# Kernel optimization log

Hardware: AMD Instinct MI355X
Metric: run time of the kernel (lower is better)

The kernel has to match this reference:

```python
import jax, jax.numpy as jnp
import numpy as np

B, S, H = 4, 2048, 2048
I = 1408          # expert intermediate size
E = 8             # num_experts
K = 2             # num_experts_per_tok


def setup_inputs() -> dict:
    key = jax.random.key(0)
    ks = jax.random.split(key, 5)
    sc_h = 1.0 / np.sqrt(H)
    sc_i = 1.0 / np.sqrt(I)
    return {
        "hidden_states": jax.random.normal(ks[0], (B, S, H), dtype=jnp.float32),
        "gate_w": jax.random.normal(ks[1], (E, H), dtype=jnp.float32) * sc_h,      # router: Linear(H, E)
        "w_gate": jax.random.normal(ks[2], (E, H, I), dtype=jnp.float32) * sc_h,   # experts_gate_proj
        "w_up": jax.random.normal(ks[3], (E, H, I), dtype=jnp.float32) * sc_h,     # experts_up_proj
        "w_down": jax.random.normal(ks[4], (E, I, H), dtype=jnp.float32) * sc_i,   # experts_down_proj
    }


def reference(hidden_states, gate_w, w_gate, w_up, w_down):
    b, s, h = hidden_states.shape
    x = hidden_states.reshape(-1, h)                       # [T, H], T = b*s
    # Router: softmax over experts, then top-k and renormalize (matches torch code).
    router_logits = x @ gate_w.T                           # [T, E]
    routing_weights = jax.nn.softmax(router_logits, axis=-1)
    topk_w, topk_i = jax.lax.top_k(routing_weights, K)     # [T, K]
    topk_w = topk_w / jnp.sum(topk_w, axis=-1, keepdims=True)
    out = jnp.zeros_like(x)
    # Loop over the small fixed expert set; tokens not routed to expert e get
    # combine weight 0, so their contribution vanishes (same math as masked gather).
    for e in range(w_gate.shape[0]):
        w_e = jnp.sum(jnp.where(topk_i == e, topk_w, 0.0), axis=-1)  # [T]
        gated = jax.nn.silu(x @ w_gate[e]) * (x @ w_up[e])           # [T, I]
        out = out + w_e[:, None] * (gated @ w_down[e])               # [T, H]
    return out.reshape(b, s, h)
```

## Files before the change

### kernel.cpp

```cpp
#include <hip/hip_runtime.h>

#define T_TOK 8192
#define H_DIM 2048
#define I_DIM 1408
#define N_EXP 8
#define MAX_TILES 144
#define R_BLOCKS 512

typedef __attribute__((ext_vector_type(8))) short short8;
typedef __attribute__((ext_vector_type(8))) unsigned short ushort8;
typedef __attribute__((ext_vector_type(4))) float f32x4;


__device__ __forceinline__ unsigned short f2bf(float f) {
  unsigned u = __float_as_uint(f);
  u += 0x7fffu + ((u >> 16) & 1u);
  return (unsigned short)(u >> 16);
}
__device__ __forceinline__ float bf2f(unsigned short u) {
  return __uint_as_float(((unsigned)u) << 16);
}

__device__ __forceinline__ void g2lds16(const unsigned short* g, unsigned short* l) {
  __builtin_amdgcn_global_load_lds(
      (const __attribute__((address_space(1))) void*)g,
      (__attribute__((address_space(3))) void*)l, 16, 0, 0);
}

__global__ __launch_bounds__(256) void router_kernel(
    const float* __restrict__ X, const float* __restrict__ GW,
    int* __restrict__ topk_e, float* __restrict__ topk_p,
    int* __restrict__ counts_blk, unsigned short* __restrict__ Xb) {
  int wave = threadIdx.x >> 6, lane = threadIdx.x & 63;
  __shared__ int hist[8];
  if (threadIdx.x < 8) hist[threadIdx.x] = 0;
  __syncthreads();

  int tok0 = blockIdx.x * 16 + wave * 4;
  const float4* g4 = (const float4*)GW;
  const float4* x4 = (const float4*)X;

  float acc[4][8];
#pragma unroll
  for (int t = 0; t < 4; t++)
#pragma unroll
    for (int e = 0; e < 8; e++) acc[t][e] = 0.f;

#pragma unroll
  for (int i = 0; i < 8; i++) {
    float4 gv[8];
#pragma unroll
    for (int e = 0; e < 8; e++) gv[e] = g4[e * 512 + lane + i * 64];
#pragma unroll
    for (int t = 0; t < 4; t++) {
      float4 xv = x4[(size_t)(tok0 + t) * 512 + lane + i * 64];
      ushort4 o;
      o.x = f2bf(xv.x); o.y = f2bf(xv.y); o.z = f2bf(xv.z); o.w = f2bf(xv.w);
      *(ushort4*)(Xb + (size_t)(tok0 + t) * H_DIM + (size_t)(lane + i * 64) * 4) = o;
#pragma unroll
      for (int e = 0; e < 8; e++)
        acc[t][e] += xv.x * gv[e].x + xv.y * gv[e].y + xv.z * gv[e].z + xv.w * gv[e].w;
    }
  }

#pragma unroll
  for (int t = 0; t < 4; t++) {
#pragma unroll
    for (int e = 0; e < 8; e++) {
      float v = acc[t][e];
      for (int off = 32; off; off >>= 1) v += __shfl_down(v, off);
      acc[t][e] = v;
    }
    if (lane == 0) {
      int token = tok0 + t;
      int e1 = 0; float l1 = acc[t][0];
#pragma unroll
      for (int e = 1; e < 8; e++) if (acc[t][e] > l1) { l1 = acc[t][e]; e1 = e; }
      int e2 = -1; float l2 = -1e30f;
#pragma unroll
      for (int e = 0; e < 8; e++) if (e != e1 && acc[t][e] > l2) { l2 = acc[t][e]; e2 = e; }
      float tt = __expf(l2 - l1);
      float p1 = 1.f / (1.f + tt);
      float p2 = tt / (1.f + tt);
      topk_e[token * 2] = e1; topk_e[token * 2 + 1] = e2;
      topk_p[token * 2] = p1; topk_p[token * 2 + 1] = p2;
      atomicAdd(&hist[e1], 1);
      atomicAdd(&hist[e2], 1);
    }
  }
  __syncthreads();
  if (threadIdx.x < 8) counts_blk[blockIdx.x * 8 + threadIdx.x] = hist[threadIdx.x];
}

__global__ __launch_bounds__(256) void setup_kernel(
    const int* __restrict__ counts_blk, int* __restrict__ cursor,
    int* __restrict__ ntiles, int* __restrict__ tile_e,
    int* __restrict__ tile_b, int* __restrict__ tile_r) {
  __shared__ int scnt[8];
  __shared__ int off[9], tb[9], cnt[8];
  int t = threadIdx.x, lane = t & 63;
  if (t < 8) scnt[t] = 0;
  __syncthreads();

  int priv[8];
#pragma unroll
  for (int e = 0; e < 8; e++) priv[e] = 0;
  for (int b = t; b < R_BLOCKS; b += 256) {
#pragma unroll
    for (int e = 0; e < 8; e++) priv[e] += counts_blk[b * 8 + e];
  }
#pragma unroll
  for (int e = 0; e < 8; e++)
    for (int o = 32; o; o >>= 1) priv[e] += __shfl_down(priv[e], o);
  if (lane == 0) {
#pragma unroll
    for (int e = 0; e < 8; e++) atomicAdd(&scnt[e], priv[e]);
  }
  __syncthreads();

  if (t == 0) {
    int o = 0, nt = 0;
    for (int e = 0; e < N_EXP; e++) {
      int n = scnt[e];
      cnt[e] = n; off[e] = o; tb[e] = nt;
      cursor[e] = o;
      nt += (n + 127) >> 7;
      o += n;
    }
    off[8] = o; tb[8] = nt;
    *ntiles = nt;
  }
  __syncthreads();
  int total = tb[8];
  for (int i = t; i < total; i += 256) {
    int e = 0;
    while (i >= tb[e + 1]) e++;
    int k = i - tb[e];
    tile_e[i] = e;
    tile_b[i] = off[e] + k * 128;
    int rem = cnt[e] - k * 128;
    tile_r[i] = rem < 128 ? rem : 128;
  }
}

__global__ __launch_bounds__(256) void scatter_kernel(
    const int* __restrict__ topk_e, int* __restrict__ cursor,
    int* __restrict__ pair_tok, int* __restrict__ slot) {
  __shared__ int lcnt[8], lbase[8];
  int tid = threadIdx.x;
  if (tid < 8) lcnt[tid] = 0;
  __syncthreads();
  int tok = blockIdx.x * 256 + tid;
  int e0 = topk_e[tok * 2], e1 = topk_e[tok * 2 + 1];
  int p0 = atomicAdd(&lcnt[e0], 1);
  int p1 = atomicAdd(&lcnt[e1], 1);
  __syncthreads();
  if (tid < 8) lbase[tid] = atomicAdd(&cursor[tid], lcnt[tid]);
  __syncthreads();
  int s0 = lbase[e0] + p0, s1 = lbase[e1] + p1;
  pair_tok[s0] = tok;
  pair_tok[s1] = tok;
  slot[tok * 2] = s0;
  slot[tok * 2 + 1] = s1;
}

__global__ __launch_bounds__(256) void transpose_cvt_kernel(
    const float* __restrict__ in, unsigned short* __restrict__ out, int R, int C) {
  __shared__ float S[64][65];
  int e = blockIdx.z;
  int c0 = blockIdx.x * 64, r0 = blockIdx.y * 64;
  const float* ine = in + (size_t)e * R * C;
  unsigned short* oute = out + (size_t)e * R * C;
  int t = threadIdx.x;
  int li = (t & 15) * 4, lr = t >> 4;
#pragma unroll
  for (int p = 0; p < 4; p++) {
    int r = lr + p * 16;
    float4 v = *(const float4*)(ine + (size_t)(r0 + r) * C + c0 + li);
    S[r][li] = v.x; S[r][li + 1] = v.y; S[r][li + 2] = v.z; S[r][li + 3] = v.w;
  }
  __syncthreads();
  int c = t >> 2, q = t & 3;
#pragma unroll
  for (int i = 0; i < 2; i++) {
    int rb = i * 32 + q * 8;
    ushort8 o;
#pragma unroll
    for (int j = 0; j < 8; j++) o[j] = f2bf(S[rb + j][c]);
    *(ushort8*)(oute + (size_t)(c0 + c) * R + r0 + rb) = o;
  }
}

__global__ __launch_bounds__(256, 2) void gemm1_kernel(
    const unsigned short* __restrict__ Xb, const unsigned short* __restrict__ Wgt,
    const unsigned short* __restrict__ Wut, const int* __restrict__ ntiles,
    const int* __restrict__ tile_e, const int* __restrict__ tile_b,
    const int* __restrict__ tile_r, const int* __restrict__ pair_tok,
    unsigned short* __restrict__ G, int tile_base) {
  int bx = blockIdx.y + tile_base;
  if (bx >= *ntiles) return;
  int e = tile_e[bx], mbase = tile_b[bx], rows = tile_r[bx];
  int n0 = blockIdx.x * 128;
  int tid = threadIdx.x, wave = tid >> 6, lane = tid & 63;
  int quad = lane >> 4, c = lane & 15;
  int wm = (wave & 1) * 64, wn = (wave >> 1) * 64;

  __shared__ __align__(16) unsigned short As[2][128][32];
  __shared__ __align__(16) unsigned short Bgs[2][128][32];
  __shared__ __align__(16) unsigned short Bus[2][128][32];

  int srow = wave * 32 + (lane >> 2);
  int selem = (lane & 3) * 8;
  int mr0 = srow < rows ? srow : 0;
  int mr1 = (srow + 16) < rows ? (srow + 16) : 0;
  const unsigned short* gA0 = Xb + (size_t)pair_tok[mbase + mr0] * H_DIM + selem;
  const unsigned short* gA1 = Xb + (size_t)pair_tok[mbase + mr1] * H_DIM + selem;
  const unsigned short* bg = Wgt + (size_t)e * H_DIM * I_DIM;
  const unsigned short* bu = Wut + (size_t)e * H_DIM * I_DIM;
  const unsigned short* gG0 = bg + (size_t)(n0 + srow) * H_DIM + selem;
  const unsigned short* gG1 = bg + (size_t)(n0 + srow + 16) * H_DIM + selem;
  const unsigned short* gU0 = bu + (size_t)(n0 + srow) * H_DIM + selem;
  const unsigned short* gU1 = bu + (size_t)(n0 + srow + 16) * H_DIM + selem;

  f32x4 accg[4][4], accu[4][4];
#pragma unroll
  for (int i = 0; i < 4; i++)
#pragma unroll
    for (int j = 0; j < 4; j++) { accg[i][j] = (f32x4)0.f; accu[i][j] = (f32x4)0.f; }

  for (int k0 = 0; k0 < H_DIM; k0 += 64) {
    __syncthreads();
#pragma unroll
    for (int s = 0; s < 2; s++) {
      int kk = k0 + s * 32;
      g2lds16(gA0 + kk, &As[s][wave * 32][0]);
      g2lds16(gA1 + kk, &As[s][wave * 32 + 16][0]);
      g2lds16(gG0 + kk, &Bgs[s][wave * 32][0]);
      g2lds16(gG1 + kk, &Bgs[s][wave * 32 + 16][0]);
      g2lds16(gU0 + kk, &Bus[s][wave * 32][0]);
      g2lds16(gU1 + kk, &Bus[s][wave * 32 + 16][0]);
    }
    __syncthreads();

#pragma unroll
    for (int h = 0; h < 2; h++) {
      short8 af[4], bgf[4], buf[4];
#pragma unroll
      for (int mt = 0; mt < 4; mt++)
        af[mt] = *(const short8*)&As[h][wm + mt * 16 + c][quad * 8];
#pragma unroll
      for (int nt = 0; nt < 4; nt++) {
        bgf[nt] = *(const short8*)&Bgs[h][wn + nt * 16 + c][quad * 8];
        buf[nt] = *(const short8*)&Bus[h][wn + nt * 16 + c][quad * 8];
      }
#pragma unroll
      for (int mt = 0; mt < 4; mt++)
#pragma unroll
        for (int nt = 0; nt < 4; nt++) {
          accg[mt][nt] = __builtin_amdgcn_mfma_f32_16x16x32_bf16(af[mt], bgf[nt], accg[mt][nt], 0, 0, 0);
          accu[mt][nt] = __builtin_amdgcn_mfma_f32_16x16x32_bf16(af[mt], buf[nt], accu[mt][nt], 0, 0, 0);
        }
    }
  }

#pragma unroll
  for (int mt = 0; mt < 4; mt++)
#pragma unroll
    for (int r = 0; r < 4; r++) {
      int m = wm + mt * 16 + quad * 4 + r;
      if (m < rows) {
        unsigned short* grow = G + (size_t)(mbase + m) * I_DIM + n0 + wn;
#pragma unroll
        for (int nt = 0; nt < 4; nt++) {
          float g = accg[mt][nt][r], u = accu[mt][nt][r];
          float val = (g / (1.f + __expf(-g))) * u;
          grow[nt * 16 + c] = f2bf(val);
        }
      }
    }
}

__global__ __launch_bounds__(256, 3) void gemm2_kernel(
    const unsigned short* __restrict__ G, const unsigned short* __restrict__ Wdt,
    const int* __restrict__ ntiles, const int* __restrict__ tile_e,
    const int* __restrict__ tile_b, const int* __restrict__ tile_r,
    unsigned short* __restrict__ Y) {
  int bx = blockIdx.y;
  if (bx >= *ntiles) return;
  int e = tile_e[bx], mbase = tile_b[bx], rows = tile_r[bx];
  int n0 = blockIdx.x * 128;
  int tid = threadIdx.x, wave = tid >> 6, lane = tid & 63;
  int quad = lane >> 4, c = lane & 15;
  int wm = (wave & 1) * 64, wn = (wave >> 1) * 64;

  __shared__ __align__(16) unsigned short As[2][128][32];
  __shared__ __align__(16) unsigned short Bs[2][128][32];

  int srow = wave * 32 + (lane >> 2);
  int selem = (lane & 3) * 8;
  int mr0 = srow < rows ? srow : 0;
  int mr1 = (srow + 16) < rows ? (srow + 16) : 0;
  const unsigned short* gA0 = G + (size_t)(mbase + mr0) * I_DIM + selem;
  const unsigned short* gA1 = G + (size_t)(mbase + mr1) * I_DIM + selem;
  const unsigned short* bd = Wdt + (size_t)e * H_DIM * I_DIM;
  const unsigned short* gB0 = bd + (size_t)(n0 + srow) * I_DIM + selem;
  const unsigned short* gB1 = bd + (size_t)(n0 + srow + 16) * I_DIM + selem;

  f32x4 acc[4][4];
#pragma unroll
  for (int i = 0; i < 4; i++)
#pragma unroll
    for (int j = 0; j < 4; j++) acc[i][j] = (f32x4)0.f;

  for (int k0 = 0; k0 < I_DIM; k0 += 64) {
    __syncthreads();
#pragma unroll
    for (int s = 0; s < 2; s++) {
      int kk = k0 + s * 32;
      g2lds16(gA0 + kk, &As[s][wave * 32][0]);
      g2lds16(gA1 + kk, &As[s][wave * 32 + 16][0]);
      g2lds16(gB0 + kk, &Bs[s][wave * 32][0]);
      g2lds16(gB1 + kk, &Bs[s][wave * 32 + 16][0]);
    }
    __syncthreads();

#pragma unroll
    for (int h = 0; h < 2; h++) {
      short8 af[4], bf[4];
#pragma unroll
      for (int mt = 0; mt < 4; mt++)
        af[mt] = *(const short8*)&As[h][wm + mt * 16 + c][quad * 8];
#pragma unroll
      for (int nt = 0; nt < 4; nt++)
        bf[nt] = *(const short8*)&Bs[h][wn + nt * 16 + c][quad * 8];
#pragma unroll
      for (int mt = 0; mt < 4; mt++)
#pragma unroll
        for (int nt = 0; nt < 4; nt++)
          acc[mt][nt] = __builtin_amdgcn_mfma_f32_16x16x32_bf16(af[mt], bf[nt], acc[mt][nt], 0, 0, 0);
    }
  }

#pragma unroll
  for (int mt = 0; mt < 4; mt++)
#pragma unroll
    for (int r = 0; r < 4; r++) {
      int m = wm + mt * 16 + quad * 4 + r;
      if (m < rows) {
        unsigned short* yrow = Y + (size_t)(mbase + m) * H_DIM + n0 + wn;
#pragma unroll
        for (int nt = 0; nt < 4; nt++) yrow[nt * 16 + c] = f2bf(acc[mt][nt][r]);
      }
    }
}

__global__ __launch_bounds__(256) void combine_kernel(
    const unsigned short* __restrict__ Y, const int* __restrict__ slot,
    const float* __restrict__ topk_p, float* __restrict__ out) {
  int t = blockIdx.x;
  int h = threadIdx.x * 8;
  int s1 = slot[t * 2], s2 = slot[t * 2 + 1];
  float p1 = topk_p[t * 2], p2 = topk_p[t * 2 + 1];
  ushort8 a = *(const ushort8*)(Y + (size_t)s1 * H_DIM + h);
  ushort8 b = *(const ushort8*)(Y + (size_t)s2 * H_DIM + h);
  float* o = out + (size_t)t * H_DIM + h;
  float4 o0, o1;
  o0.x = p1 * bf2f(a[0]) + p2 * bf2f(b[0]);
  o0.y = p1 * bf2f(a[1]) + p2 * bf2f(b[1]);
  o0.z = p1 * bf2f(a[2]) + p2 * bf2f(b[2]);
  o0.w = p1 * bf2f(a[3]) + p2 * bf2f(b[3]);
  o1.x = p1 * bf2f(a[4]) + p2 * bf2f(b[4]);
  o1.y = p1 * bf2f(a[5]) + p2 * bf2f(b[5]);
  o1.z = p1 * bf2f(a[6]) + p2 * bf2f(b[6]);
  o1.w = p1 * bf2f(a[7]) + p2 * bf2f(b[7]);
  *(float4*)o = o0;
  *(float4*)(o + 4) = o1;
}

extern "C" void kernel_launch(void* const* d_in, const int* in_sizes, int n_in,
                              void* d_out, int out_size, void* d_ws, size_t ws_size,
                              hipStream_t stream) {
  const float* X  = (const float*)d_in[0];
  const float* GW = (const float*)d_in[1];
  const float* Wg = (const float*)d_in[2];
  const float* Wu = (const float*)d_in[3];
  const float* Wd = (const float*)d_in[4];
  float* out = (float*)d_out;

  char* ws = (char*)d_ws;
  int*   cursor   = (int*)(ws + 32);
  int*   ntiles   = (int*)(ws + 64);
  int*   tile_e   = (int*)(ws + 128);
  int*   tile_b   = (int*)(ws + 1280);
  int*   tile_r   = (int*)(ws + 2432);
  int*   topk_e   = (int*)(ws + 4096);
  float* topk_p   = (float*)(ws + 69632);
  int*   pair_tok = (int*)(ws + 135168);
  int*   slot     = (int*)(ws + 200704);
  int*   counts_blk = (int*)(ws + 200704);
  unsigned short* Xb  = (unsigned short*)(ws + 266240);
  unsigned short* G   = (unsigned short*)(ws + 33820672);
  unsigned short* Wgt = (unsigned short*)(ws + 79958016);
  unsigned short* Wut = (unsigned short*)(ws + 126095360);
  unsigned short* Wdt = (unsigned short*)(ws + 172232704);
  unsigned short* Y   = (unsigned short*)(ws + 79958016);


  router_kernel<<<R_BLOCKS, 256, 0, stream>>>(X, GW, topk_e, topk_p, counts_blk, Xb);
  setup_kernel<<<1, 256, 0, stream>>>(counts_blk, cursor, ntiles, tile_e, tile_b, tile_r);
  scatter_kernel<<<T_TOK / 256, 256, 0, stream>>>(topk_e, cursor, pair_tok, slot);
  transpose_cvt_kernel<<<dim3(I_DIM / 64, H_DIM / 64, N_EXP), 256, 0, stream>>>(Wg, Wgt, H_DIM, I_DIM);
  transpose_cvt_kernel<<<dim3(I_DIM / 64, H_DIM / 64, N_EXP), 256, 0, stream>>>(Wu, Wut, H_DIM, I_DIM);
  transpose_cvt_kernel<<<dim3(H_DIM / 64, I_DIM / 64, N_EXP), 256, 0, stream>>>(Wd, Wdt, I_DIM, H_DIM);

  gemm1_kernel<<<dim3(I_DIM / 128, MAX_TILES), 256, 0, stream>>>(
      Xb, Wgt, Wut, ntiles, tile_e, tile_b, tile_r, pair_tok, G, 0);
  gemm2_kernel<<<dim3(H_DIM / 128, MAX_TILES), 256, 0, stream>>>(
      G, Wdt, ntiles, tile_e, tile_b, tile_r, Y);
  combine_kernel<<<T_TOK, 256, 0, stream>>>(Y, slot, topk_p, out);
}
```

Baseline: 746.9 us.

## Remap GEMM workgroups across XCDs for L2 reuse and merge weight transposes

The GEMM grids are flattened to 1D. Block ids are remapped so that consecutive logical tiles, which share the same token tile and expert weights, land on the same XCD of the MI355X. The aim is better L2 reuse of the A rows and expert weights, which the default round-robin dispatch scatters across chiplets. The three weight transpose/convert launches are also merged into one launch with a 24-slice grid, cutting launch overhead and the tail idle time between kernels. Because of the remap, early-exit blocks for unused tiles are now spread across all XCDs rather than bunched at the end of the grid.

```diff
diff --git a/kernel.cpp b/kernel.cpp
--- a/kernel.cpp
+++ b/kernel.cpp
@@ -6,6 +6,11 @@
 #define N_EXP 8
 #define MAX_TILES 144
 #define R_BLOCKS 512
+
+#define GRID1 (11 * MAX_TILES)
+#define CHUNK1 (GRID1 / 8)
+#define GRID2 (16 * MAX_TILES)
+#define CHUNK2 (GRID2 / 8)
 
 typedef __attribute__((ext_vector_type(8))) short short8;
 typedef __attribute__((ext_vector_type(8))) unsigned short ushort8;
@@ -164,13 +169,21 @@
   slot[tok * 2 + 1] = s1;
 }
 
-__global__ __launch_bounds__(256) void transpose_cvt_kernel(
-    const float* __restrict__ in, unsigned short* __restrict__ out, int R, int C) {
+__global__ __launch_bounds__(256) void transpose_cvt_all_kernel(
+    const float* __restrict__ Wg, const float* __restrict__ Wu,
+    const float* __restrict__ Wd, unsigned short* __restrict__ Wgt,
+    unsigned short* __restrict__ Wut, unsigned short* __restrict__ Wdt) {
   __shared__ float S[64][65];
-  int e = blockIdx.z;
-  int c0 = blockIdx.x * 64, r0 = blockIdx.y * 64;
-  const float* ine = in + (size_t)e * R * C;
-  unsigned short* oute = out + (size_t)e * R * C;
+  int z = blockIdx.y;
+  const float* in; unsigned short* out; int R, C, e;
+  if (z < 8)       { in = Wg; out = Wgt; R = H_DIM; C = I_DIM; e = z; }
+  else if (z < 16) { in = Wu; out = Wut; R = H_DIM; C = I_DIM; e = z - 8; }
+  else             { in = Wd; out = Wdt; R = I_DIM; C = H_DIM; e = z - 16; }
+  int nx = C >> 6;
+  int bid = blockIdx.x;
+  int c0 = (bid % nx) * 64, r0 = (bid / nx) * 64;
+  const float* ine = in + (size_t)e * H_DIM * I_DIM;
+  unsigned short* oute = out + (size_t)e * H_DIM * I_DIM;
   int t = threadIdx.x;
   int li = (t & 15) * 4, lr = t >> 4;
 #pragma unroll
@@ -196,11 +209,13 @@
     const unsigned short* __restrict__ Wut, const int* __restrict__ ntiles,
     const int* __restrict__ tile_e, const int* __restrict__ tile_b,
     const int* __restrict__ tile_r, const int* __restrict__ pair_tok,
-    unsigned short* __restrict__ G, int tile_base) {
-  int bx = blockIdx.y + tile_base;
+    unsigned short* __restrict__ G) {
+  int orig = blockIdx.x;
+  int wg = (orig & 7) * CHUNK1 + (orig >> 3);
+  int bx = wg / 11;
   if (bx >= *ntiles) return;
+  int n0 = (wg - bx * 11) * 128;
   int e = tile_e[bx], mbase = tile_b[bx], rows = tile_r[bx];
-  int n0 = blockIdx.x * 128;
   int tid = threadIdx.x, wave = tid >> 6, lane = tid & 63;
   int quad = lane >> 4, c = lane & 15;
   int wm = (wave & 1) * 64, wn = (wave >> 1) * 64;
@@ -285,10 +300,12 @@
     const int* __restrict__ ntiles, const int* __restrict__ tile_e,
     const int* __restrict__ tile_b, const int* __restrict__ tile_r,
     unsigned short* __restrict__ Y) {
-  int bx = blockIdx.y;
+  int orig = blockIdx.x;
+  int wg = (orig & 7) * CHUNK2 + (orig >> 3);
+  int bx = wg >> 4;
   if (bx >= *ntiles) return;
+  int n0 = (wg & 15) * 128;
   int e = tile_e[bx], mbase = tile_b[bx], rows = tile_r[bx];
-  int n0 = blockIdx.x * 128;
   int tid = threadIdx.x, wave = tid >> 6, lane = tid & 63;
   int quad = lane >> 4, c = lane & 15;
   int wm = (wave & 1) * 64, wn = (wave >> 1) * 64;
@@ -405,17 +422,14 @@
   unsigned short* Wdt = (unsigned short*)(ws + 172232704);
   unsigned short* Y   = (unsigned short*)(ws + 79958016);
 
-
   router_kernel<<<R_BLOCKS, 256, 0, stream>>>(X, GW, topk_e, topk_p, counts_blk, Xb);
   setup_kernel<<<1, 256, 0, stream>>>(counts_blk, cursor, ntiles, tile_e, tile_b, tile_r);
   scatter_kernel<<<T_TOK / 256, 256, 0, stream>>>(topk_e, cursor, pair_tok, slot);
-  transpose_cvt_kernel<<<dim3(I_DIM / 64, H_DIM / 64, N_EXP), 256, 0, stream>>>(Wg, Wgt, H_DIM, I_DIM);
-  transpose_cvt_kernel<<<dim3(I_DIM / 64, H_DIM / 64, N_EXP), 256, 0, stream>>>(Wu, Wut, H_DIM, I_DIM);
-  transpose_cvt_kernel<<<dim3(H_DIM / 64, I_DIM / 64, N_EXP), 256, 0, stream>>>(Wd, Wdt, I_DIM, H_DIM);
-
-  gemm1_kernel<<<dim3(I_DIM / 128, MAX_TILES), 256, 0, stream>>>(
-      Xb, Wgt, Wut, ntiles, tile_e, tile_b, tile_r, pair_tok, G, 0);
-  gemm2_kernel<<<dim3(H_DIM / 128, MAX_TILES), 256, 0, stream>>>(
+  transpose_cvt_all_kernel<<<dim3(704, 24), 256, 0, stream>>>(Wg, Wu, Wd, Wgt, Wut, Wdt);
+
+  gemm1_kernel<<<GRID1, 256, 0, stream>>>(
+      Xb, Wgt, Wut, ntiles, tile_e, tile_b, tile_r, pair_tok, G);
+  gemm2_kernel<<<GRID2, 256, 0, stream>>>(
       G, Wdt, ntiles, tile_e, tile_b, tile_r, Y);
   combine_kernel<<<T_TOK, 256, 0, stream>>>(Y, slot, topk_p, out);
 }
```

Result: slower. 779.1 us (+4.3%).

## Use 256x256 tiles with interleaved gate/up weights and pipelined swizzled LDS

Applied to the files above, without the earlier changes.

The expert GEMMs move from 128x128 tiles with 4 waves to 256x256 tiles with 8 waves, 64-wide K steps, XOR-swizzled LDS and a staggered prefetch pipeline with barriers and s_setprio. The gate and up weights are interleaved into one W1 matrix in 16-row groups so a single B operand feeds both accumulators. The three weight transposes are fused into one launch, and block indices are remapped so the 8 blocks sharing a weight tile run together. This aims to raise arithmetic intensity and MFMA utilisation, at the cost of more padding waste on partial expert tiles and more register pressure.

```diff
diff --git a/kernel.cpp b/kernel.cpp
--- a/kernel.cpp
+++ b/kernel.cpp
@@ -4,8 +4,11 @@
 #define H_DIM 2048
 #define I_DIM 1408
 #define N_EXP 8
-#define MAX_TILES 144
+#define MAX_T2 72
 #define R_BLOCKS 512
+
+#define G1_GRID (MAX_T2 * 11)
+#define G2_GRID (MAX_T2 * 8)
 
 typedef __attribute__((ext_vector_type(8))) short short8;
 typedef __attribute__((ext_vector_type(8))) unsigned short ushort8;
@@ -124,7 +127,7 @@
       int n = scnt[e];
       cnt[e] = n; off[e] = o; tb[e] = nt;
       cursor[e] = o;
-      nt += (n + 127) >> 7;
+      nt += (n + 255) >> 8;
       o += n;
     }
     off[8] = o; tb[8] = nt;
@@ -137,9 +140,9 @@
     while (i >= tb[e + 1]) e++;
     int k = i - tb[e];
     tile_e[i] = e;
-    tile_b[i] = off[e] + k * 128;
-    int rem = cnt[e] - k * 128;
-    tile_r[i] = rem < 128 ? rem : 128;
+    tile_b[i] = off[e] + k * 256;
+    int rem = cnt[e] - k * 256;
+    tile_r[i] = rem < 256 ? rem : 256;
   }
 }
 
@@ -164,192 +167,316 @@
   slot[tok * 2 + 1] = s1;
 }
 
-__global__ __launch_bounds__(256) void transpose_cvt_kernel(
-    const float* __restrict__ in, unsigned short* __restrict__ out, int R, int C) {
+__global__ __launch_bounds__(256) void transpose_cvt_all_kernel(
+    const float* __restrict__ Wg, const float* __restrict__ Wu,
+    const float* __restrict__ Wd, unsigned short* __restrict__ W1,
+    unsigned short* __restrict__ Wdt) {
   __shared__ float S[64][65];
-  int e = blockIdx.z;
-  int c0 = blockIdx.x * 64, r0 = blockIdx.y * 64;
-  const float* ine = in + (size_t)e * R * C;
-  unsigned short* oute = out + (size_t)e * R * C;
+  int z = blockIdx.y;
+  const float* in; unsigned short* outp; int C, s = 0;
+  if (z < 16) {
+    s = (z >> 3) & 1;
+    int e = z & 7;
+    in = (s ? Wu : Wg) + (size_t)e * H_DIM * I_DIM;
+    outp = W1 + (size_t)e * 2816 * H_DIM;
+    C = I_DIM;
+  } else {
+    int e = z - 16;
+    in = Wd + (size_t)e * H_DIM * I_DIM;
+    outp = Wdt + (size_t)e * H_DIM * I_DIM;
+    C = H_DIM;
+  }
+  int nx = C >> 6;
+  int c0 = (blockIdx.x % nx) * 64, r0 = (blockIdx.x / nx) * 64;
   int t = threadIdx.x;
   int li = (t & 15) * 4, lr = t >> 4;
 #pragma unroll
   for (int p = 0; p < 4; p++) {
     int r = lr + p * 16;
-    float4 v = *(const float4*)(ine + (size_t)(r0 + r) * C + c0 + li);
+    float4 v = *(const float4*)(in + (size_t)(r0 + r) * C + c0 + li);
     S[r][li] = v.x; S[r][li + 1] = v.y; S[r][li + 2] = v.z; S[r][li + 3] = v.w;
   }
   __syncthreads();
   int c = t >> 2, q = t & 3;
+  size_t orow;
+  if (z < 16) {
+    int cc2 = c0 + c;
+    orow = (size_t)((cc2 >> 4) * 32 + s * 16 + (cc2 & 15)) * H_DIM;
+  } else {
+    orow = (size_t)(c0 + c) * I_DIM;
+  }
 #pragma unroll
   for (int i = 0; i < 2; i++) {
     int rb = i * 32 + q * 8;
     ushort8 o;
 #pragma unroll
     for (int j = 0; j < 8; j++) o[j] = f2bf(S[rb + j][c]);
-    *(ushort8*)(oute + (size_t)(c0 + c) * R + r0 + rb) = o;
-  }
-}
-
-__global__ __launch_bounds__(256, 2) void gemm1_kernel(
-    const unsigned short* __restrict__ Xb, const unsigned short* __restrict__ Wgt,
-    const unsigned short* __restrict__ Wut, const int* __restrict__ ntiles,
-    const int* __restrict__ tile_e, const int* __restrict__ tile_b,
-    const int* __restrict__ tile_r, const int* __restrict__ pair_tok,
-    unsigned short* __restrict__ G, int tile_base) {
-  int bx = blockIdx.y + tile_base;
+    *(ushort8*)(outp + orow + r0 + rb) = o;
+  }
+}
+
+
+__global__ __launch_bounds__(512, 2) void gemm1_kernel(
+    const unsigned short* __restrict__ Xb, const unsigned short* __restrict__ W1,
+    const int* __restrict__ ntiles, const int* __restrict__ tile_e,
+    const int* __restrict__ tile_b, const int* __restrict__ tile_r,
+    const int* __restrict__ pair_tok, unsigned short* __restrict__ G) {
+  int x = blockIdx.x & 7, jj0 = blockIdx.x >> 3;
+  int bx = x + 8 * (jj0 / 11);
   if (bx >= *ntiles) return;
+  int n0 = (jj0 % 11) * 256;
   int e = tile_e[bx], mbase = tile_b[bx], rows = tile_r[bx];
-  int n0 = blockIdx.x * 128;
-  int tid = threadIdx.x, wave = tid >> 6, lane = tid & 63;
-  int quad = lane >> 4, c = lane & 15;
-  int wm = (wave & 1) * 64, wn = (wave >> 1) * 64;
-
-  __shared__ __align__(16) unsigned short As[2][128][32];
-  __shared__ __align__(16) unsigned short Bgs[2][128][32];
-  __shared__ __align__(16) unsigned short Bus[2][128][32];
-
-  int srow = wave * 32 + (lane >> 2);
-  int selem = (lane & 3) * 8;
-  int mr0 = srow < rows ? srow : 0;
-  int mr1 = (srow + 16) < rows ? (srow + 16) : 0;
-  const unsigned short* gA0 = Xb + (size_t)pair_tok[mbase + mr0] * H_DIM + selem;
-  const unsigned short* gA1 = Xb + (size_t)pair_tok[mbase + mr1] * H_DIM + selem;
-  const unsigned short* bg = Wgt + (size_t)e * H_DIM * I_DIM;
-  const unsigned short* bu = Wut + (size_t)e * H_DIM * I_DIM;
-  const unsigned short* gG0 = bg + (size_t)(n0 + srow) * H_DIM + selem;
-  const unsigned short* gG1 = bg + (size_t)(n0 + srow + 16) * H_DIM + selem;
-  const unsigned short* gU0 = bu + (size_t)(n0 + srow) * H_DIM + selem;
-  const unsigned short* gU1 = bu + (size_t)(n0 + srow + 16) * H_DIM + selem;
-
-  f32x4 accg[4][4], accu[4][4];
-#pragma unroll
-  for (int i = 0; i < 4; i++)
-#pragma unroll
-    for (int j = 0; j < 4; j++) { accg[i][j] = (f32x4)0.f; accu[i][j] = (f32x4)0.f; }
-
-  for (int k0 = 0; k0 < H_DIM; k0 += 64) {
-    __syncthreads();
-#pragma unroll
-    for (int s = 0; s < 2; s++) {
-      int kk = k0 + s * 32;
-      g2lds16(gA0 + kk, &As[s][wave * 32][0]);
-      g2lds16(gA1 + kk, &As[s][wave * 32 + 16][0]);
-      g2lds16(gG0 + kk, &Bgs[s][wave * 32][0]);
-      g2lds16(gG1 + kk, &Bgs[s][wave * 32 + 16][0]);
-      g2lds16(gU0 + kk, &Bus[s][wave * 32][0]);
-      g2lds16(gU1 + kk, &Bus[s][wave * 32 + 16][0]);
-    }
-    __syncthreads();
-
-#pragma unroll
-    for (int h = 0; h < 2; h++) {
-      short8 af[4], bgf[4], buf[4];
-#pragma unroll
-      for (int mt = 0; mt < 4; mt++)
-        af[mt] = *(const short8*)&As[h][wm + mt * 16 + c][quad * 8];
-#pragma unroll
-      for (int nt = 0; nt < 4; nt++) {
-        bgf[nt] = *(const short8*)&Bgs[h][wn + nt * 16 + c][quad * 8];
-        buf[nt] = *(const short8*)&Bus[h][wn + nt * 16 + c][quad * 8];
-      }
-#pragma unroll
-      for (int mt = 0; mt < 4; mt++)
-#pragma unroll
-        for (int nt = 0; nt < 4; nt++) {
-          accg[mt][nt] = __builtin_amdgcn_mfma_f32_16x16x32_bf16(af[mt], bgf[nt], accg[mt][nt], 0, 0, 0);
-          accu[mt][nt] = __builtin_amdgcn_mfma_f32_16x16x32_bf16(af[mt], buf[nt], accu[mt][nt], 0, 0, 0);
-        }
-    }
-  }
-
-#pragma unroll
-  for (int mt = 0; mt < 4; mt++)
-#pragma unroll
-    for (int r = 0; r < 4; r++) {
+
+  int tid = threadIdx.x, wid = tid >> 6, lane = tid & 63;
+  int cc = lane & 15, quad = lane >> 4;
+  int wm = (wid >> 2) * 128, wn = (wid & 3) * 64;
+  int lr = lane >> 3;
+  int koff = ((lane & 7) ^ (lr & 7)) * 8;
+
+  __shared__ __align__(16) unsigned short As[2][256][64];
+  __shared__ __align__(16) unsigned short Bs[2][256][64];
+
+  const unsigned short* w1e = W1 + (size_t)e * 2816 * H_DIM;
+  const unsigned short* aS[2][2];
+  const unsigned short* bS[2][2];
+#pragma unroll
+  for (int h = 0; h < 2; ++h)
+#pragma unroll
+    for (int ld = 0; ld < 2; ++ld) {
+      int r = h * 128 + wid * 16 + ld * 8 + lr;
+      int mr = r < rows ? r : 0;
+      aS[h][ld] = Xb + (size_t)pair_tok[mbase + mr] * H_DIM + koff;
+      bS[h][ld] = w1e + (size_t)(n0 + r) * H_DIM + koff;
+    }
+
+  f32x4 acc[8][4];
+#pragma unroll
+  for (int i = 0; i < 8; ++i)
+#pragma unroll
+    for (int j = 0; j < 4; ++j) acc[i][j] = (f32x4)0.f;
+
+  int rcol[2];
+  rcol[0] = (quad * 8) ^ ((cc & 7) * 8);
+  rcol[1] = (32 + quad * 8) ^ ((cc & 7) * 8);
+
+#pragma unroll
+  for (int h = 0; h < 2; ++h) {
+    g2lds16(aS[h][0], &As[0][h * 128 + wid * 16][0]);
+    g2lds16(aS[h][1], &As[0][h * 128 + wid * 16 + 8][0]);
+  }
+#pragma unroll
+  for (int h = 0; h < 2; ++h) {
+    g2lds16(bS[h][0], &Bs[0][h * 128 + wid * 16][0]);
+    g2lds16(bS[h][1], &Bs[0][h * 128 + wid * 16 + 8][0]);
+  }
+#pragma unroll
+  for (int h = 0; h < 2; ++h) {
+    g2lds16(bS[h][0] + 64, &Bs[1][h * 128 + wid * 16][0]);
+    g2lds16(bS[h][1] + 64, &Bs[1][h * 128 + wid * 16 + 8][0]);
+  }
+  asm volatile("s_waitcnt vmcnt(4)" ::: "memory");
+  __builtin_amdgcn_s_barrier();
+
+  const int NT = H_DIM / 64;
+  for (int t = 0; t < NT; ++t) {
+    int cb = t & 1, nb = cb ^ 1;
+    int k1 = (t + 1) * 64, k2 = (t + 2) * 64;
+    short8 bf[4][2];
+#pragma unroll
+    for (int p = 0; p < 4; ++p) {
+      if (p == 0 && t + 1 < NT) {
+        g2lds16(aS[0][0] + k1, &As[nb][wid * 16][0]);
+        g2lds16(aS[0][1] + k1, &As[nb][wid * 16 + 8][0]);
+      }
+      if (p == 1 && t + 1 < NT) {
+        g2lds16(aS[1][0] + k1, &As[nb][128 + wid * 16][0]);
+        g2lds16(aS[1][1] + k1, &As[nb][128 + wid * 16 + 8][0]);
+      }
+      if (p == 2 && t + 2 < NT) {
+        g2lds16(bS[0][0] + k2, &Bs[cb][wid * 16][0]);
+        g2lds16(bS[0][1] + k2, &Bs[cb][wid * 16 + 8][0]);
+      }
+      if (p == 3 && t + 2 < NT) {
+        g2lds16(bS[1][0] + k2, &Bs[cb][128 + wid * 16][0]);
+        g2lds16(bS[1][1] + k2, &Bs[cb][128 + wid * 16 + 8][0]);
+      }
+      asm volatile("" ::: "memory");
+      if (p == 0) {
+#pragma unroll
+        for (int nt = 0; nt < 4; ++nt)
+#pragma unroll
+          for (int ks = 0; ks < 2; ++ks)
+            bf[nt][ks] = *(const short8*)&Bs[cb][wn + nt * 16 + cc][rcol[ks]];
+      }
+      short8 af[2][2];
+#pragma unroll
+      for (int j = 0; j < 2; ++j)
+#pragma unroll
+        for (int ks = 0; ks < 2; ++ks)
+          af[j][ks] = *(const short8*)&As[cb][wm + (2 * p + j) * 16 + cc][rcol[ks]];
+      if (p == 3) {
+        if (t == NT - 2) asm volatile("s_waitcnt vmcnt(0)" ::: "memory");
+        else if (t < NT - 2) asm volatile("s_waitcnt vmcnt(4)" ::: "memory");
+      }
+      __builtin_amdgcn_s_barrier();
+      __builtin_amdgcn_s_setprio(1);
+#pragma unroll
+      for (int j = 0; j < 2; ++j)
+#pragma unroll
+        for (int nt = 0; nt < 4; ++nt)
+#pragma unroll
+          for (int ks = 0; ks < 2; ++ks)
+            acc[2 * p + j][nt] = __builtin_amdgcn_mfma_f32_16x16x32_bf16(
+                af[j][ks], bf[nt][ks], acc[2 * p + j][nt], 0, 0, 0);
+      __builtin_amdgcn_s_setprio(0);
+      __builtin_amdgcn_s_barrier();
+    }
+  }
+
+  int ibase = ((n0 + wn) >> 5) * 16 + cc;
+#pragma unroll
+  for (int mt = 0; mt < 8; ++mt)
+#pragma unroll
+    for (int r = 0; r < 4; ++r) {
       int m = wm + mt * 16 + quad * 4 + r;
       if (m < rows) {
-        unsigned short* grow = G + (size_t)(mbase + m) * I_DIM + n0 + wn;
-#pragma unroll
-        for (int nt = 0; nt < 4; nt++) {
-          float g = accg[mt][nt][r], u = accu[mt][nt][r];
+        unsigned short* grow = G + (size_t)(mbase + m) * I_DIM + ibase;
+#pragma unroll
+        for (int pp = 0; pp < 2; ++pp) {
+          float g = acc[mt][2 * pp][r], u = acc[mt][2 * pp + 1][r];
           float val = (g / (1.f + __expf(-g))) * u;
-          grow[nt * 16 + c] = f2bf(val);
+          grow[pp * 16] = f2bf(val);
         }
       }
     }
 }
 
-__global__ __launch_bounds__(256, 3) void gemm2_kernel(
+__global__ __launch_bounds__(512, 2) void gemm2_kernel(
     const unsigned short* __restrict__ G, const unsigned short* __restrict__ Wdt,
     const int* __restrict__ ntiles, const int* __restrict__ tile_e,
     const int* __restrict__ tile_b, const int* __restrict__ tile_r,
     unsigned short* __restrict__ Y) {
-  int bx = blockIdx.y;
+  int x = blockIdx.x & 7, jj0 = blockIdx.x >> 3;
+  int bx = x + 8 * (jj0 >> 3);
   if (bx >= *ntiles) return;
+  int n0 = (jj0 & 7) * 256;
   int e = tile_e[bx], mbase = tile_b[bx], rows = tile_r[bx];
-  int n0 = blockIdx.x * 128;
-  int tid = threadIdx.x, wave = tid >> 6, lane = tid & 63;
-  int quad = lane >> 4, c = lane & 15;
-  int wm = (wave & 1) * 64, wn = (wave >> 1) * 64;
-
-  __shared__ __align__(16) unsigned short As[2][128][32];
-  __shared__ __align__(16) unsigned short Bs[2][128][32];
-
-  int srow = wave * 32 + (lane >> 2);
-  int selem = (lane & 3) * 8;
-  int mr0 = srow < rows ? srow : 0;
-  int mr1 = (srow + 16) < rows ? (srow + 16) : 0;
-  const unsigned short* gA0 = G + (size_t)(mbase + mr0) * I_DIM + selem;
-  const unsigned short* gA1 = G + (size_t)(mbase + mr1) * I_DIM + selem;
-  const unsigned short* bd = Wdt + (size_t)e * H_DIM * I_DIM;
-  const unsigned short* gB0 = bd + (size_t)(n0 + srow) * I_DIM + selem;
-  const unsigned short* gB1 = bd + (size_t)(n0 + srow + 16) * I_DIM + selem;
-
-  f32x4 acc[4][4];
-#pragma unroll
-  for (int i = 0; i < 4; i++)
-#pragma unroll
-    for (int j = 0; j < 4; j++) acc[i][j] = (f32x4)0.f;
-
-  for (int k0 = 0; k0 < I_DIM; k0 += 64) {
-    __syncthreads();
-#pragma unroll
-    for (int s = 0; s < 2; s++) {
-      int kk = k0 + s * 32;
-      g2lds16(gA0 + kk, &As[s][wave * 32][0]);
-      g2lds16(gA1 + kk, &As[s][wave * 32 + 16][0]);
-      g2lds16(gB0 + kk, &Bs[s][wave * 32][0]);
-      g2lds16(gB1 + kk, &Bs[s][wave * 32 + 16][0]);
-    }
-    __syncthreads();
-
-#pragma unroll
-    for (int h = 0; h < 2; h++) {
-      short8 af[4], bf[4];
-#pragma unroll
-      for (int mt = 0; mt < 4; mt++)
-        af[mt] = *(const short8*)&As[h][wm + mt * 16 + c][quad * 8];
-#pragma unroll
-      for (int nt = 0; nt < 4; nt++)
-        bf[nt] = *(const short8*)&Bs[h][wn + nt * 16 + c][quad * 8];
-#pragma unroll
-      for (int mt = 0; mt < 4; mt++)
-#pragma unroll
-        for (int nt = 0; nt < 4; nt++)
-          acc[mt][nt] = __builtin_amdgcn_mfma_f32_16x16x32_bf16(af[mt], bf[nt], acc[mt][nt], 0, 0, 0);
-    }
-  }
-
-#pragma unroll
-  for (int mt = 0; mt < 4; mt++)
-#pragma unroll
-    for (int r = 0; r < 4; r++) {
+
+  int tid = threadIdx.x, wid = tid >> 6, lane = tid & 63;
+  int cc = lane & 15, quad = lane >> 4;
+  int wm = (wid >> 2) * 128, wn = (wid & 3) * 64;
+  int lr = lane >> 3;
+  int koff = ((lane & 7) ^ (lr & 7)) * 8;
+
+  __shared__ __align__(16) unsigned short As[2][256][64];
+  __shared__ __align__(16) unsigned short Bs[2][256][64];
+
+  const unsigned short* wde = Wdt + (size_t)e * H_DIM * I_DIM;
+  const unsigned short* aS[2][2];
+  const unsigned short* bS[2][2];
+#pragma unroll
+  for (int h = 0; h < 2; ++h)
+#pragma unroll
+    for (int ld = 0; ld < 2; ++ld) {
+      int r = h * 128 + wid * 16 + ld * 8 + lr;
+      int mr = r < rows ? r : 0;
+      aS[h][ld] = G + (size_t)(mbase + mr) * I_DIM + koff;
+      bS[h][ld] = wde + (size_t)(n0 + r) * I_DIM + koff;
+    }
+
+  f32x4 acc[8][4];
+#pragma unroll
+  for (int i = 0; i < 8; ++i)
+#pragma unroll
+    for (int j = 0; j < 4; ++j) acc[i][j] = (f32x4)0.f;
+
+  int rcol[2];
+  rcol[0] = (quad * 8) ^ ((cc & 7) * 8);
+  rcol[1] = (32 + quad * 8) ^ ((cc & 7) * 8);
+
+#pragma unroll
+  for (int h = 0; h < 2; ++h) {
+    g2lds16(aS[h][0], &As[0][h * 128 + wid * 16][0]);
+    g2lds16(aS[h][1], &As[0][h * 128 + wid * 16 + 8][0]);
+  }
+#pragma unroll
+  for (int h = 0; h < 2; ++h) {
+    g2lds16(bS[h][0], &Bs[0][h * 128 + wid * 16][0]);
+    g2lds16(bS[h][1], &Bs[0][h * 128 + wid * 16 + 8][0]);
+  }
+#pragma unroll
+  for (int h = 0; h < 2; ++h) {
+    g2lds16(bS[h][0] + 64, &Bs[1][h * 128 + wid * 16][0]);
+    g2lds16(bS[h][1] + 64, &Bs[1][h * 128 + wid * 16 + 8][0]);
+  }
+  asm volatile("s_waitcnt vmcnt(4)" ::: "memory");
+  __builtin_amdgcn_s_barrier();
+
+  const int NT = I_DIM / 64;
+  for (int t = 0; t < NT; ++t) {
+    int cb = t & 1, nb = cb ^ 1;
+    int k1 = (t + 1) * 64, k2 = (t + 2) * 64;
+    short8 bf[4][2];
+#pragma unroll
+    for (int p = 0; p < 4; ++p) {
+      if (p == 0 && t + 1 < NT) {
+        g2lds16(aS[0][0] + k1, &As[nb][wid * 16][0]);
+        g2lds16(aS[0][1] + k1, &As[nb][wid * 16 + 8][0]);
+      }
+      if (p == 1 && t + 1 < NT) {
+        g2lds16(aS[1][0] + k1, &As[nb][128 + wid * 16][0]);
+        g2lds16(aS[1][1] + k1, &As[nb][128 + wid * 16 + 8][0]);
+      }
+      if (p == 2 && t + 2 < NT) {
+        g2lds16(bS[0][0] + k2, &Bs[cb][wid * 16][0]);
+        g2lds16(bS[0][1] + k2, &Bs[cb][wid * 16 + 8][0]);
+      }
+      if (p == 3 && t + 2 < NT) {
+        g2lds16(bS[1][0] + k2, &Bs[cb][128 + wid * 16][0]);
+        g2lds16(bS[1][1] + k2, &Bs[cb][128 + wid * 16 + 8][0]);
+      }
+      asm volatile("" ::: "memory");
+      if (p == 0) {
+#pragma unroll
+        for (int nt = 0; nt < 4; ++nt)
+#pragma unroll
+          for (int ks = 0; ks < 2; ++ks)
+            bf[nt][ks] = *(const short8*)&Bs[cb][wn + nt * 16 + cc][rcol[ks]];
+      }
+      short8 af[2][2];
+#pragma unroll
+      for (int j = 0; j < 2; ++j)
+#pragma unroll
+        for (int ks = 0; ks < 2; ++ks)
+          af[j][ks] = *(const short8*)&As[cb][wm + (2 * p + j) * 16 + cc][rcol[ks]];
+      if (p == 3) {
+        if (t == NT - 2) asm volatile("s_waitcnt vmcnt(0)" ::: "memory");
+        else if (t < NT - 2) asm volatile("s_waitcnt vmcnt(4)" ::: "memory");
+      }
+      __builtin_amdgcn_s_barrier();
+      __builtin_amdgcn_s_setprio(1);
+#pragma unroll
+      for (int j = 0; j < 2; ++j)
+#pragma unroll
+        for (int nt = 0; nt < 4; ++nt)
+#pragma unroll
+          for (int ks = 0; ks < 2; ++ks)
+            acc[2 * p + j][nt] = __builtin_amdgcn_mfma_f32_16x16x32_bf16(
+                af[j][ks], bf[nt][ks], acc[2 * p + j][nt], 0, 0, 0);
+      __builtin_amdgcn_s_setprio(0);
+      __builtin_amdgcn_s_barrier();
+    }
+  }
+
+#pragma unroll
+  for (int mt = 0; mt < 8; ++mt)
+#pragma unroll
+    for (int r = 0; r < 4; ++r) {
       int m = wm + mt * 16 + quad * 4 + r;
       if (m < rows) {
         unsigned short* yrow = Y + (size_t)(mbase + m) * H_DIM + n0 + wn;
 #pragma unroll
-        for (int nt = 0; nt < 4; nt++) yrow[nt * 16 + c] = f2bf(acc[mt][nt][r]);
+        for (int nt = 0; nt < 4; ++nt) yrow[nt * 16 + cc] = f2bf(acc[mt][nt][r]);
       }
     }
 }
@@ -400,22 +527,18 @@
   int*   counts_blk = (int*)(ws + 200704);
   unsigned short* Xb  = (unsigned short*)(ws + 266240);
   unsigned short* G   = (unsigned short*)(ws + 33820672);
-  unsigned short* Wgt = (unsigned short*)(ws + 79958016);
-  unsigned short* Wut = (unsigned short*)(ws + 126095360);
+  unsigned short* W1  = (unsigned short*)(ws + 79958016);
   unsigned short* Wdt = (unsigned short*)(ws + 172232704);
   unsigned short* Y   = (unsigned short*)(ws + 79958016);
-
 
   router_kernel<<<R_BLOCKS, 256, 0, stream>>>(X, GW, topk_e, topk_p, counts_blk, Xb);
   setup_kernel<<<1, 256, 0, stream>>>(counts_blk, cursor, ntiles, tile_e, tile_b, tile_r);
   scatter_kernel<<<T_TOK / 256, 256, 0, stream>>>(topk_e, cursor, pair_tok, slot);
-  transpose_cvt_kernel<<<dim3(I_DIM / 64, H_DIM / 64, N_EXP), 256, 0, stream>>>(Wg, Wgt, H_DIM, I_DIM);
-  transpose_cvt_kernel<<<dim3(I_DIM / 64, H_DIM / 64, N_EXP), 256, 0, stream>>>(Wu, Wut, H_DIM, I_DIM);
-  transpose_cvt_kernel<<<dim3(H_DIM / 64, I_DIM / 64, N_EXP), 256, 0, stream>>>(Wd, Wdt, I_DIM, H_DIM);
-
-  gemm1_kernel<<<dim3(I_DIM / 128, MAX_TILES), 256, 0, stream>>>(
-      Xb, Wgt, Wut, ntiles, tile_e, tile_b, tile_r, pair_tok, G, 0);
-  gemm2_kernel<<<dim3(H_DIM / 128, MAX_TILES), 256, 0, stream>>>(
+  transpose_cvt_all_kernel<<<dim3(704, 24), 256, 0, stream>>>(Wg, Wu, Wd, W1, Wdt);
+
+  gemm1_kernel<<<G1_GRID, 512, 0, stream>>>(
+      Xb, W1, ntiles, tile_e, tile_b, tile_r, pair_tok, G);
+  gemm2_kernel<<<G2_GRID, 512, 0, stream>>>(
       G, Wdt, ntiles, tile_e, tile_b, tile_r, Y);
   combine_kernel<<<T_TOK, 256, 0, stream>>>(Y, slot, topk_p, out);
 }
```

Result: slower. 1.003 ms (+34.2%).
